# Kernel optimization log

Measured on AMD Instinct MI355X. Metric: run time of the kernel, lower is better.

## Reference

```python
import jax, jax.numpy as jnp
import numpy as np

B, N, H, NH = 4, 2048, 1024, 16
HD = H // NH  # head_dim = 64


def setup_inputs() -> dict:
    key = jax.random.key(0)
    k1, k2, k3 = jax.random.split(key, 3)
    s = 1.0 / np.sqrt(H)
    return {
        "x": jax.random.normal(k1, (B, N, H), dtype=jnp.float32),
        "w_qkv": jax.random.normal(k2, (3 * H, H), dtype=jnp.float32) * s,
        "b_qkv": jnp.zeros((3 * H,), dtype=jnp.float32),
        "w_out": jax.random.normal(k3, (H, H), dtype=jnp.float32) * s,
        "b_out": jnp.zeros((H,), dtype=jnp.float32),
    }


def reference(x, w_qkv, b_qkv, w_out, b_out):
    b, n, h = x.shape
    qkv = x @ w_qkv.T + b_qkv  # [b, n, 3h]
    q, k, v = jnp.split(qkv, 3, axis=-1)
    # [b, n, h] -> [b, nh, n, hd]
    def heads(t):
        return t.reshape(b, n, NH, HD).transpose(0, 2, 1, 3)
    q, k, v = heads(q), heads(k), heads(v)
    scale = HD ** -0.5
    dots = jnp.einsum('bhqd,bhkd->bhqk', q, k) * scale
    attn = jax.nn.softmax(dots, axis=-1)
    out = jnp.einsum('bhqk,bhkd->bhqd', attn, v)
    out = out.transpose(0, 2, 1, 3).reshape(b, n, h)
    return out @ w_out.T + b_out
```

## Files before the change

### kernel.cpp

```cpp
#include <hip/hip_runtime.h>

typedef __bf16 bf16x8 __attribute__((ext_vector_type(8)));
typedef float f32x4 __attribute__((ext_vector_type(4)));
typedef float f32x16 __attribute__((ext_vector_type(16)));
typedef unsigned int uint2v __attribute__((ext_vector_type(2)));

#define LOG2E 1.44269504088896340736f

#if __has_builtin(__builtin_amdgcn_exp2f)
#define EXP2(x) __builtin_amdgcn_exp2f(x)
#else
#define EXP2(x) exp2f(x)
#endif

static __device__ __forceinline__ unsigned short f2bf(float f) {
    unsigned int u = __builtin_bit_cast(unsigned int, f);
    u += 0x7fffu + ((u >> 16) & 1u);
    return (unsigned short)(u >> 16);
}

static __device__ __forceinline__ void plswap(unsigned int& a, unsigned int& b) {
#if __has_builtin(__builtin_amdgcn_permlane32_swap)
    uint2v r = __builtin_amdgcn_permlane32_swap(a, b, false, false);
    a = r.x; b = r.y;
#else
    asm("v_permlane32_swap_b32 %0, %1" : "+v"(a), "+v"(b));
#endif
}

static __device__ __forceinline__ float xhalf_add(float x) {
    unsigned int a = __builtin_bit_cast(unsigned int, x), b = a;
    plswap(a, b);
    return __builtin_bit_cast(float, a) + __builtin_bit_cast(float, b);
}

__global__ void cvt3_kernel(const float* __restrict__ x, const float* __restrict__ wq,
                            const float* __restrict__ wo,
                            unsigned short* __restrict__ xb, unsigned short* __restrict__ wqb,
                            unsigned short* __restrict__ wob) {
    int i = blockIdx.x * blockDim.x + threadIdx.x;
    int stride = gridDim.x * blockDim.x;
    for (; i < 3145728; i += stride) {
        const float* src;
        unsigned short* dst;
        int j;
        if (i < 2097152)      { j = i;           src = x;  dst = xb;  }
        else if (i < 2883584) { j = i - 2097152; src = wq; dst = wqb; }
        else                  { j = i - 2883584; src = wo; dst = wob; }
        float4 v = reinterpret_cast<const float4*>(src)[j];
        ushort4 o;
        o.x = f2bf(v.x); o.y = f2bf(v.y); o.z = f2bf(v.z); o.w = f2bf(v.w);
        reinterpret_cast<ushort4*>(dst)[j] = o;
    }
}

template <int MODE>
__global__ __launch_bounds__(256, 2) void gemm_bt(const unsigned short* __restrict__ A,
                                                  const unsigned short* __restrict__ B,
                                                  const float* __restrict__ bias,
                                                  void* __restrict__ Cout,
                                                  int M, int N, int K) {
    __shared__ unsigned short SH[2][2][128 * 64];
    const int tid = threadIdx.x;
    const int w = tid >> 6, lane = tid & 63;
    const int wr = w >> 1, wc = w & 1;
    const int bm0 = blockIdx.y << 7, bn0 = blockIdx.x << 7;
    const int l15 = lane & 15, l4 = lane >> 4;

    const int srow = w * 8 + (lane >> 3);
    const int gch = (lane & 7) ^ (lane >> 3);

    f32x4 acc[4][4] = {};

    auto stage = [&](int buf, int kt) {
        const int k0 = kt << 6;
        #pragma unroll
        for (int i = 0; i < 4; ++i) {
            int row = i * 32 + srow;
            const unsigned short* ga = A + (size_t)(bm0 + row) * K + k0 + gch * 8;
            __builtin_amdgcn_global_load_lds(
                (const __attribute__((address_space(1))) void*)ga,
                (__attribute__((address_space(3))) void*)&SH[buf][0][i * 2048 + w * 512],
                16, 0, 0);
            const unsigned short* gb = B + (size_t)(bn0 + row) * K + k0 + gch * 8;
            __builtin_amdgcn_global_load_lds(
                (const __attribute__((address_space(1))) void*)gb,
                (__attribute__((address_space(3))) void*)&SH[buf][1][i * 2048 + w * 512],
                16, 0, 0);
        }
    };

    const int nk = K >> 6;
    stage(0, 0);
    __syncthreads();
    int buf = 0;
    for (int kt = 0; kt < nk; ++kt) {
        if (kt + 1 < nk) stage(buf ^ 1, kt + 1);
        const unsigned short* as = &SH[buf][0][0];
        const unsigned short* bs = &SH[buf][1][0];
        #pragma unroll
        for (int s = 0; s < 2; ++s) {
            bf16x8 af[4], bfr[4];
            #pragma unroll
            for (int t = 0; t < 4; ++t) {
                int rowa = wr * 64 + t * 16 + l15;
                int cha = (s * 4 + l4) ^ (rowa & 7);
                af[t] = *(const bf16x8*)&as[rowa * 64 + cha * 8];
                int rowb = wc * 64 + t * 16 + l15;
                int chb = (s * 4 + l4) ^ (rowb & 7);
                bfr[t] = *(const bf16x8*)&bs[rowb * 64 + chb * 8];
            }
            #pragma unroll
            for (int i = 0; i < 4; ++i)
                #pragma unroll
                for (int j = 0; j < 4; ++j)
                    acc[i][j] = __builtin_amdgcn_mfma_f32_16x16x32_bf16(af[i], bfr[j], acc[i][j], 0, 0, 0);
        }
        __syncthreads();
        buf ^= 1;
    }

    if (MODE == 0) {
        unsigned short* O = (unsigned short*)Cout;
        if (bn0 >= 2048) {
            unsigned short* T = &SH[0][0][0];
            __syncthreads();
            #pragma unroll
            for (int j = 0; j < 4; ++j) {
                int cl = wc * 64 + j * 16 + l15;
                float bv = bias[bn0 + cl];
                #pragma unroll
                for (int i = 0; i < 4; ++i) {
                    int nl = wr * 64 + i * 16 + l4 * 4;
                    ushort4 pk;
                    pk.x = f2bf(acc[i][j][0] + bv);
                    pk.y = f2bf(acc[i][j][1] + bv);
                    pk.z = f2bf(acc[i][j][2] + bv);
                    pk.w = f2bf(acc[i][j][3] + bv);
                    *(ushort4*)&T[cl * 136 + nl] = pk;
                }
            }
            __syncthreads();
            const int b = bm0 >> 11, n0 = bm0 & 2047;
            const int h0 = (bn0 >> 6) & 15;
            #pragma unroll
            for (int it = 0; it < 8; ++it) {
                int dl = it * 16 + (tid >> 4);
                int ch = tid & 15;
                uint4 val = *(const uint4*)&T[dl * 136 + ch * 8];
                size_t idx = (size_t)16777216 +
                             ((size_t)((b * 16 + (h0 + (dl >> 6))) * 64 + (dl & 63))) * 2048 +
                             n0 + ch * 8;
                *(uint4*)&O[idx] = val;
            }
        } else {
            #pragma unroll
            for (int j = 0; j < 4; ++j) {
                int col = bn0 + wc * 64 + j * 16 + l15;
                float bv = bias[col];
                int which = col >> 10;
                int h = (col >> 6) & 15;
                int d = col & 63;
                #pragma unroll
                for (int i = 0; i < 4; ++i) {
                    #pragma unroll
                    for (int r = 0; r < 4; ++r) {
                        int row = bm0 + wr * 64 + i * 16 + l4 * 4 + r;
                        int b = row >> 11, n = row & 2047;
                        float v = acc[i][j][r] + bv;
                        size_t idx;
                        if (which == 0) { v *= 0.125f * LOG2E; idx = ((size_t)((b * 16 + h) * 2048 + n)) * 64 + d; }
                        else { idx = (size_t)8388608 + ((size_t)((b * 16 + h) * 2048 + n)) * 64 + d; }
                        O[idx] = f2bf(v);
                    }
                }
            }
        }
    } else {
        float* C = (float*)Cout;
        #pragma unroll
        for (int j = 0; j < 4; ++j) {
            int col = bn0 + wc * 64 + j * 16 + l15;
            float bv = bias[col];
            #pragma unroll
            for (int i = 0; i < 4; ++i) {
                #pragma unroll
                for (int r = 0; r < 4; ++r) {
                    int row = bm0 + wr * 64 + i * 16 + l4 * 4 + r;
                    C[(size_t)row * N + col] = acc[i][j][r] + bv;
                }
            }
        }
    }
}

__global__ __launch_bounds__(256, 2) void attn_kernel(const unsigned short* __restrict__ qkv,
                                                      unsigned short* __restrict__ out) {
    __shared__ unsigned short Klds[2][4096];
    __shared__ unsigned short Vlds[2][4096];

    const int tid = threadIdx.x;
    const int w = tid >> 6, lane = tid & 63;
    const int ql = lane & 31;
    const int hi = lane >> 5;
    const int id = blockIdx.x;
    const int bh = id & 63;
    const int qt = id >> 6;
    const size_t SEC = 8388608;

    const unsigned short* Q  = qkv + (size_t)bh * (2048 * 64);
    const unsigned short* Kp = qkv + SEC + (size_t)bh * (2048 * 64);
    const unsigned short* Vt = qkv + 2 * SEC + (size_t)bh * (64 * 2048);

    const int q0 = qt * 256 + w * 64;

    bf16x8 qbA[4], qbB[4];
    #pragma unroll
    for (int c = 0; c < 4; ++c) {
        qbA[c] = *(const bf16x8*)&Q[(size_t)(q0 + ql) * 64 + c * 16 + hi * 8];
        qbB[c] = *(const bf16x8*)&Q[(size_t)(q0 + 32 + ql) * 64 + c * 16 + hi * 8];
    }

    f32x16 oA0 = {}, oA1 = {}, oB0 = {}, oB1 = {};
    float lsA = 0.f, lsB = 0.f;

    const int sri = lane >> 3;
    const int sch = lane & 7;

    auto stage = [&](int buf, int tile) {
        const int kb = tile * 64;
        #pragma unroll
        for (int i = 0; i < 2; ++i) {
            const int r = w * 16 + i * 8 + sri;
            const int c = sch ^ (r & 7);
            const unsigned short* gk = Kp + (size_t)(kb + r) * 64 + c * 8;
            __builtin_amdgcn_global_load_lds(
                (const __attribute__((address_space(1))) void*)gk,
                (__attribute__((address_space(3))) void*)&Klds[buf][w * 1024 + i * 512],
                16, 0, 0);
            const unsigned short* gv = Vt + (size_t)r * 2048 + kb + c * 8;
            __builtin_amdgcn_global_load_lds(
                (const __attribute__((address_space(1))) void*)gv,
                (__attribute__((address_space(3))) void*)&Vlds[buf][w * 1024 + i * 512],
                16, 0, 0);
        }
    };

    auto softmax_block = [&](f32x16& s0, f32x16& s1, float& lsum,
                             bf16x8 (&p0)[2], bf16x8 (&p1)[2]) {
        #pragma unroll
        for (int r = 0; r < 16; ++r) s0[r] = EXP2(s0[r]);
        #pragma unroll
        for (int r = 0; r < 16; ++r) s1[r] = EXP2(s1[r]);
        float u0 = ((s0[0] + s0[1]) + (s0[2] + s0[3])) + ((s0[4] + s0[5]) + (s0[6] + s0[7]));
        float u1 = ((s0[8] + s0[9]) + (s0[10] + s0[11])) + ((s0[12] + s0[13]) + (s0[14] + s0[15]));
        float u2 = ((s1[0] + s1[1]) + (s1[2] + s1[3])) + ((s1[4] + s1[5]) + (s1[6] + s1[7]));
        float u3 = ((s1[8] + s1[9]) + (s1[10] + s1[11])) + ((s1[12] + s1[13]) + (s1[14] + s1[15]));
        float rs = (u0 + u1) + (u2 + u3);
        lsum += xhalf_add(rs);
        #pragma unroll
        for (int g = 0; g < 2; ++g) {
            unsigned int x0, x1, x2, x3;
            asm("v_cvt_pk_bf16_f32 %0, %1, %2" : "=v"(x0) : "v"(s0[8*g + 0]), "v"(s0[8*g + 1]));
            asm("v_cvt_pk_bf16_f32 %0, %1, %2" : "=v"(x1) : "v"(s0[8*g + 2]), "v"(s0[8*g + 3]));
            asm("v_cvt_pk_bf16_f32 %0, %1, %2" : "=v"(x2) : "v"(s0[8*g + 4]), "v"(s0[8*g + 5]));
            asm("v_cvt_pk_bf16_f32 %0, %1, %2" : "=v"(x3) : "v"(s0[8*g + 6]), "v"(s0[8*g + 7]));
            plswap(x0, x2);
            plswap(x1, x3);
            uint4 wds; wds.x = x0; wds.y = x1; wds.z = x2; wds.w = x3;
            p0[g] = __builtin_bit_cast(bf16x8, wds);
        }
        #pragma unroll
        for (int g = 0; g < 2; ++g) {
            unsigned int x0, x1, x2, x3;
            asm("v_cvt_pk_bf16_f32 %0, %1, %2" : "=v"(x0) : "v"(s1[8*g + 0]), "v"(s1[8*g + 1]));
            asm("v_cvt_pk_bf16_f32 %0, %1, %2" : "=v"(x1) : "v"(s1[8*g + 2]), "v"(s1[8*g + 3]));
            asm("v_cvt_pk_bf16_f32 %0, %1, %2" : "=v"(x2) : "v"(s1[8*g + 4]), "v"(s1[8*g + 5]));
            asm("v_cvt_pk_bf16_f32 %0, %1, %2" : "=v"(x3) : "v"(s1[8*g + 6]), "v"(s1[8*g + 7]));
            plswap(x0, x2);
            plswap(x1, x3);
            uint4 wds; wds.x = x0; wds.y = x1; wds.z = x2; wds.w = x3;
            p1[g] = __builtin_bit_cast(bf16x8, wds);
        }
    };

    stage(0, 0);
    __syncthreads();

    for (int t = 0; t < 32; ++t) {
        const int cur = t & 1;
        if (t + 1 < 32) stage(cur ^ 1, t + 1);

        bf16x8 k0[4], k1[4];
        #pragma unroll
        for (int mf = 0; mf < 4; ++mf) {
            int c0 = ((mf * 2 + hi) ^ (ql & 7));
            k0[mf] = *(const bf16x8*)&Klds[cur][ql * 64 + c0 * 8];
            k1[mf] = *(const bf16x8*)&Klds[cur][(32 + ql) * 64 + c0 * 8];
        }

        f32x16 sA0 = {}, sA1 = {};
        #pragma unroll
        for (int mf = 0; mf < 4; ++mf)
            sA0 = __builtin_amdgcn_mfma_f32_32x32x16_bf16(k0[mf], qbA[mf], sA0, 0, 0, 0);
        #pragma unroll
        for (int mf = 0; mf < 4; ++mf)
            sA1 = __builtin_amdgcn_mfma_f32_32x32x16_bf16(k1[mf], qbA[mf], sA1, 0, 0, 0);
        f32x16 sB0 = {}, sB1 = {};
        #pragma unroll
        for (int mf = 0; mf < 4; ++mf)
            sB0 = __builtin_amdgcn_mfma_f32_32x32x16_bf16(k0[mf], qbB[mf], sB0, 0, 0, 0);
        #pragma unroll
        for (int mf = 0; mf < 4; ++mf)
            sB1 = __builtin_amdgcn_mfma_f32_32x32x16_bf16(k1[mf], qbB[mf], sB1, 0, 0, 0);

        bf16x8 v0[4], v1[4];
        #pragma unroll
        for (int ks = 0; ks < 4; ++ks) {
            int c0 = ((ks * 2 + hi) ^ (ql & 7));
            v0[ks] = *(const bf16x8*)&Vlds[cur][ql * 64 + c0 * 8];
            v1[ks] = *(const bf16x8*)&Vlds[cur][(32 + ql) * 64 + c0 * 8];
        }

        bf16x8 pA0[2], pA1[2], pB0[2], pB1[2];
        softmax_block(sA0, sA1, lsA, pA0, pA1);
        softmax_block(sB0, sB1, lsB, pB0, pB1);

        oA0 = __builtin_amdgcn_mfma_f32_32x32x16_bf16(v0[0], pA0[0], oA0, 0, 0, 0);
        oA0 = __builtin_amdgcn_mfma_f32_32x32x16_bf16(v0[1], pA0[1], oA0, 0, 0, 0);
        oA0 = __builtin_amdgcn_mfma_f32_32x32x16_bf16(v0[2], pA1[0], oA0, 0, 0, 0);
        oA0 = __builtin_amdgcn_mfma_f32_32x32x16_bf16(v0[3], pA1[1], oA0, 0, 0, 0);
        oA1 = __builtin_amdgcn_mfma_f32_32x32x16_bf16(v1[0], pA0[0], oA1, 0, 0, 0);
        oA1 = __builtin_amdgcn_mfma_f32_32x32x16_bf16(v1[1], pA0[1], oA1, 0, 0, 0);
        oA1 = __builtin_amdgcn_mfma_f32_32x32x16_bf16(v1[2], pA1[0], oA1, 0, 0, 0);
        oA1 = __builtin_amdgcn_mfma_f32_32x32x16_bf16(v1[3], pA1[1], oA1, 0, 0, 0);
        oB0 = __builtin_amdgcn_mfma_f32_32x32x16_bf16(v0[0], pB0[0], oB0, 0, 0, 0);
        oB0 = __builtin_amdgcn_mfma_f32_32x32x16_bf16(v0[1], pB0[1], oB0, 0, 0, 0);
        oB0 = __builtin_amdgcn_mfma_f32_32x32x16_bf16(v0[2], pB1[0], oB0, 0, 0, 0);
        oB0 = __builtin_amdgcn_mfma_f32_32x32x16_bf16(v0[3], pB1[1], oB0, 0, 0, 0);
        oB1 = __builtin_amdgcn_mfma_f32_32x32x16_bf16(v1[0], pB0[0], oB1, 0, 0, 0);
        oB1 = __builtin_amdgcn_mfma_f32_32x32x16_bf16(v1[1], pB0[1], oB1, 0, 0, 0);
        oB1 = __builtin_amdgcn_mfma_f32_32x32x16_bf16(v1[2], pB1[0], oB1, 0, 0, 0);
        oB1 = __builtin_amdgcn_mfma_f32_32x32x16_bf16(v1[3], pB1[1], oB1, 0, 0, 0);

        __syncthreads();
    }

    const int b = bh >> 4, h = bh & 15;
    {
        const float inv = 1.0f / lsA;
        const int n = q0 + ql;
        unsigned short* obase = out + ((size_t)(b * 2048 + n)) * 1024 + h * 64;
        #pragma unroll
        for (int g = 0; g < 4; ++g) {
            int d0 = 8 * g + 4 * hi;
            ushort4 w0, w1;
            w0.x = f2bf(oA0[4 * g + 0] * inv);
            w0.y = f2bf(oA0[4 * g + 1] * inv);
            w0.z = f2bf(oA0[4 * g + 2] * inv);
            w0.w = f2bf(oA0[4 * g + 3] * inv);
            *(ushort4*)(obase + d0) = w0;
            w1.x = f2bf(oA1[4 * g + 0] * inv);
            w1.y = f2bf(oA1[4 * g + 1] * inv);
            w1.z = f2bf(oA1[4 * g + 2] * inv);
            w1.w = f2bf(oA1[4 * g + 3] * inv);
            *(ushort4*)(obase + 32 + d0) = w1;
        }
    }
    {
        const float inv = 1.0f / lsB;
        const int n = q0 + 32 + ql;
        unsigned short* obase = out + ((size_t)(b * 2048 + n)) * 1024 + h * 64;
        #pragma unroll
        for (int g = 0; g < 4; ++g) {
            int d0 = 8 * g + 4 * hi;
            ushort4 w0, w1;
            w0.x = f2bf(oB0[4 * g + 0] * inv);
            w0.y = f2bf(oB0[4 * g + 1] * inv);
            w0.z = f2bf(oB0[4 * g + 2] * inv);
            w0.w = f2bf(oB0[4 * g + 3] * inv);
            *(ushort4*)(obase + d0) = w0;
            w1.x = f2bf(oB1[4 * g + 0] * inv);
            w1.y = f2bf(oB1[4 * g + 1] * inv);
            w1.z = f2bf(oB1[4 * g + 2] * inv);
            w1.w = f2bf(oB1[4 * g + 3] * inv);
            *(ushort4*)(obase + 32 + d0) = w1;
        }
    }
}

extern "C" void kernel_launch(void* const* d_in, const int* in_sizes, int n_in,
                              void* d_out, int out_size, void* d_ws, size_t ws_size,
                              hipStream_t stream) {
    (void)in_sizes; (void)n_in; (void)out_size; (void)ws_size;
    const float* x     = (const float*)d_in[0];
    const float* w_qkv = (const float*)d_in[1];
    const float* b_qkv = (const float*)d_in[2];
    const float* w_out = (const float*)d_in[3];
    const float* b_out = (const float*)d_in[4];

    unsigned short* ws = (unsigned short*)d_ws;
    unsigned short* xb    = ws;
    unsigned short* wqkvb = ws + 8388608;
    unsigned short* woutb = ws + 11534336;
    unsigned short* qkvb  = ws + 12582912;

    cvt3_kernel<<<dim3(2048), dim3(256), 0, stream>>>(x, w_qkv, w_out, xb, wqkvb, woutb);

    gemm_bt<0><<<dim3(24, 64), dim3(256), 0, stream>>>(xb, wqkvb, b_qkv, (void*)qkvb, 8192, 3072, 1024);

    attn_kernel<<<dim3(512), dim3(256), 0, stream>>>(qkvb, xb);

    gemm_bt<1><<<dim3(8, 64), dim3(256), 0, stream>>>(xb, woutb, b_out, d_out, 8192, 1024, 1024);
}
```

Measured before the change: 176.0 us.

## Split attention work across 8 waves with 32 query rows each

The attention block grows from 256 to 512 threads, so each wave handles 32 query rows instead of 64. Each wave holds half the Q fragments and accumulators, which lowers register pressure and allows more waves per CU for latency hiding. K/V staging is spread over 8 waves with one load each. The cost is that every wave reads the full K/V tile from LDS for half the math, doubling LDS read traffic per MFMA, and the barrier now covers more waves.

New measurement: 178.5 us. Within noise of the previous version (+1.4%).

```diff
diff --git a/kernel.cpp b/kernel.cpp
--- a/kernel.cpp
+++ b/kernel.cpp
@@ -194,7 +194,7 @@
     }
 }
 
-__global__ __launch_bounds__(256, 2) void attn_kernel(const unsigned short* __restrict__ qkv,
+__global__ __launch_bounds__(512, 4) void attn_kernel(const unsigned short* __restrict__ qkv,
                                                       unsigned short* __restrict__ out) {
     __shared__ unsigned short Klds[2][4096];
     __shared__ unsigned short Vlds[2][4096];
@@ -212,42 +212,66 @@
     const unsigned short* Kp = qkv + SEC + (size_t)bh * (2048 * 64);
     const unsigned short* Vt = qkv + 2 * SEC + (size_t)bh * (64 * 2048);
 
-    const int q0 = qt * 256 + w * 64;
-
-    bf16x8 qbA[4], qbB[4];
+    const int q0 = qt * 256 + w * 32;
+
+    bf16x8 qb[4];
     #pragma unroll
-    for (int c = 0; c < 4; ++c) {
-        qbA[c] = *(const bf16x8*)&Q[(size_t)(q0 + ql) * 64 + c * 16 + hi * 8];
-        qbB[c] = *(const bf16x8*)&Q[(size_t)(q0 + 32 + ql) * 64 + c * 16 + hi * 8];
-    }
-
-    f32x16 oA0 = {}, oA1 = {}, oB0 = {}, oB1 = {};
-    float lsA = 0.f, lsB = 0.f;
+    for (int c = 0; c < 4; ++c)
+        qb[c] = *(const bf16x8*)&Q[(size_t)(q0 + ql) * 64 + c * 16 + hi * 8];
+
+    f32x16 o0 = {}, o1 = {};
+    float ls = 0.f;
 
     const int sri = lane >> 3;
     const int sch = lane & 7;
 
     auto stage = [&](int buf, int tile) {
         const int kb = tile * 64;
-        #pragma unroll
-        for (int i = 0; i < 2; ++i) {
-            const int r = w * 16 + i * 8 + sri;
-            const int c = sch ^ (r & 7);
-            const unsigned short* gk = Kp + (size_t)(kb + r) * 64 + c * 8;
-            __builtin_amdgcn_global_load_lds(
-                (const __attribute__((address_space(1))) void*)gk,
-                (__attribute__((address_space(3))) void*)&Klds[buf][w * 1024 + i * 512],
-                16, 0, 0);
-            const unsigned short* gv = Vt + (size_t)r * 2048 + kb + c * 8;
-            __builtin_amdgcn_global_load_lds(
-                (const __attribute__((address_space(1))) void*)gv,
-                (__attribute__((address_space(3))) void*)&Vlds[buf][w * 1024 + i * 512],
-                16, 0, 0);
-        }
+        const int r = w * 8 + sri;
+        const int c = sch ^ (r & 7);
+        const unsigned short* gk = Kp + (size_t)(kb + r) * 64 + c * 8;
+        __builtin_amdgcn_global_load_lds(
+            (const __attribute__((address_space(1))) void*)gk,
+            (__attribute__((address_space(3))) void*)&Klds[buf][w * 512],
+            16, 0, 0);
+        const unsigned short* gv = Vt + (size_t)r * 2048 + kb + c * 8;
+        __builtin_amdgcn_global_load_lds(
+            (const __attribute__((address_space(1))) void*)gv,
+            (__attribute__((address_space(3))) void*)&Vlds[buf][w * 512],
+            16, 0, 0);
     };
 
-    auto softmax_block = [&](f32x16& s0, f32x16& s1, float& lsum,
-                             bf16x8 (&p0)[2], bf16x8 (&p1)[2]) {
+    stage(0, 0);
+    __syncthreads();
+
+    for (int t = 0; t < 32; ++t) {
+        const int cur = t & 1;
+        if (t + 1 < 32) stage(cur ^ 1, t + 1);
+
+        bf16x8 k0[4], k1[4];
+        #pragma unroll
+        for (int mf = 0; mf < 4; ++mf) {
+            int c0 = ((mf * 2 + hi) ^ (ql & 7));
+            k0[mf] = *(const bf16x8*)&Klds[cur][ql * 64 + c0 * 8];
+            k1[mf] = *(const bf16x8*)&Klds[cur][(32 + ql) * 64 + c0 * 8];
+        }
+
+        f32x16 s0 = {}, s1 = {};
+        #pragma unroll
+        for (int mf = 0; mf < 4; ++mf)
+            s0 = __builtin_amdgcn_mfma_f32_32x32x16_bf16(k0[mf], qb[mf], s0, 0, 0, 0);
+        #pragma unroll
+        for (int mf = 0; mf < 4; ++mf)
+            s1 = __builtin_amdgcn_mfma_f32_32x32x16_bf16(k1[mf], qb[mf], s1, 0, 0, 0);
+
+        bf16x8 v0[4], v1[4];
+        #pragma unroll
+        for (int ks = 0; ks < 4; ++ks) {
+            int c0 = ((ks * 2 + hi) ^ (ql & 7));
+            v0[ks] = *(const bf16x8*)&Vlds[cur][ql * 64 + c0 * 8];
+            v1[ks] = *(const bf16x8*)&Vlds[cur][(32 + ql) * 64 + c0 * 8];
+        }
+
         #pragma unroll
         for (int r = 0; r < 16; ++r) s0[r] = EXP2(s0[r]);
         #pragma unroll
@@ -257,7 +281,9 @@
         float u2 = ((s1[0] + s1[1]) + (s1[2] + s1[3])) + ((s1[4] + s1[5]) + (s1[6] + s1[7]));
         float u3 = ((s1[8] + s1[9]) + (s1[10] + s1[11])) + ((s1[12] + s1[13]) + (s1[14] + s1[15]));
         float rs = (u0 + u1) + (u2 + u3);
-        lsum += xhalf_add(rs);
+        ls += xhalf_add(rs);
+
+        bf16x8 p0[2], p1[2];
         #pragma unroll
         for (int g = 0; g < 2; ++g) {
             unsigned int x0, x1, x2, x3;
@@ -282,110 +308,37 @@
             uint4 wds; wds.x = x0; wds.y = x1; wds.z = x2; wds.w = x3;
             p1[g] = __builtin_bit_cast(bf16x8, wds);
         }
-    };
-
-    stage(0, 0);
-    __syncthreads();
-
-    for (int t = 0; t < 32; ++t) {
-        const int cur = t & 1;
-        if (t + 1 < 32) stage(cur ^ 1, t + 1);
-
-        bf16x8 k0[4], k1[4];
-        #pragma unroll
-        for (int mf = 0; mf < 4; ++mf) {
-            int c0 = ((mf * 2 + hi) ^ (ql & 7));
-            k0[mf] = *(const bf16x8*)&Klds[cur][ql * 64 + c0 * 8];
-            k1[mf] = *(const bf16x8*)&Klds[cur][(32 + ql) * 64 + c0 * 8];
-        }
-
-        f32x16 sA0 = {}, sA1 = {};
-        #pragma unroll
-        for (int mf = 0; mf < 4; ++mf)
-            sA0 = __builtin_amdgcn_mfma_f32_32x32x16_bf16(k0[mf], qbA[mf], sA0, 0, 0, 0);
-        #pragma unroll
-        for (int mf = 0; mf < 4; ++mf)
-            sA1 = __builtin_amdgcn_mfma_f32_32x32x16_bf16(k1[mf], qbA[mf], sA1, 0, 0, 0);
-        f32x16 sB0 = {}, sB1 = {};
-        #pragma unroll
-        for (int mf = 0; mf < 4; ++mf)
-            sB0 = __builtin_amdgcn_mfma_f32_32x32x16_bf16(k0[mf], qbB[mf], sB0, 0, 0, 0);
-        #pragma unroll
-        for (int mf = 0; mf < 4; ++mf)
-            sB1 = __builtin_amdgcn_mfma_f32_32x32x16_bf16(k1[mf], qbB[mf], sB1, 0, 0, 0);
-
-        bf16x8 v0[4], v1[4];
-        #pragma unroll
-        for (int ks = 0; ks < 4; ++ks) {
-            int c0 = ((ks * 2 + hi) ^ (ql & 7));
-            v0[ks] = *(const bf16x8*)&Vlds[cur][ql * 64 + c0 * 8];
-            v1[ks] = *(const bf16x8*)&Vlds[cur][(32 + ql) * 64 + c0 * 8];
-        }
-
-        bf16x8 pA0[2], pA1[2], pB0[2], pB1[2];
-        softmax_block(sA0, sA1, lsA, pA0, pA1);
-        softmax_block(sB0, sB1, lsB, pB0, pB1);
-
-        oA0 = __builtin_amdgcn_mfma_f32_32x32x16_bf16(v0[0], pA0[0], oA0, 0, 0, 0);
-        oA0 = __builtin_amdgcn_mfma_f32_32x32x16_bf16(v0[1], pA0[1], oA0, 0, 0, 0);
-        oA0 = __builtin_amdgcn_mfma_f32_32x32x16_bf16(v0[2], pA1[0], oA0, 0, 0, 0);
-        oA0 = __builtin_amdgcn_mfma_f32_32x32x16_bf16(v0[3], pA1[1], oA0, 0, 0, 0);
-        oA1 = __builtin_amdgcn_mfma_f32_32x32x16_bf16(v1[0], pA0[0], oA1, 0, 0, 0);
-        oA1 = __builtin_amdgcn_mfma_f32_32x32x16_bf16(v1[1], pA0[1], oA1, 0, 0, 0);
-        oA1 = __builtin_amdgcn_mfma_f32_32x32x16_bf16(v1[2], pA1[0], oA1, 0, 0, 0);
-        oA1 = __builtin_amdgcn_mfma_f32_32x32x16_bf16(v1[3], pA1[1], oA1, 0, 0, 0);
-        oB0 = __builtin_amdgcn_mfma_f32_32x32x16_bf16(v0[0], pB0[0], oB0, 0, 0, 0);
-        oB0 = __builtin_amdgcn_mfma_f32_32x32x16_bf16(v0[1], pB0[1], oB0, 0, 0, 0);
-        oB0 = __builtin_amdgcn_mfma_f32_32x32x16_bf16(v0[2], pB1[0], oB0, 0, 0, 0);
-        oB0 = __builtin_amdgcn_mfma_f32_32x32x16_bf16(v0[3], pB1[1], oB0, 0, 0, 0);
-        oB1 = __builtin_amdgcn_mfma_f32_32x32x16_bf16(v1[0], pB0[0], oB1, 0, 0, 0);
-        oB1 = __builtin_amdgcn_mfma_f32_32x32x16_bf16(v1[1], pB0[1], oB1, 0, 0, 0);
-        oB1 = __builtin_amdgcn_mfma_f32_32x32x16_bf16(v1[2], pB1[0], oB1, 0, 0, 0);
-        oB1 = __builtin_amdgcn_mfma_f32_32x32x16_bf16(v1[3], pB1[1], oB1, 0, 0, 0);
+
+        o0 = __builtin_amdgcn_mfma_f32_32x32x16_bf16(v0[0], p0[0], o0, 0, 0, 0);
+        o0 = __builtin_amdgcn_mfma_f32_32x32x16_bf16(v0[1], p0[1], o0, 0, 0, 0);
+        o0 = __builtin_amdgcn_mfma_f32_32x32x16_bf16(v0[2], p1[0], o0, 0, 0, 0);
+        o0 = __builtin_amdgcn_mfma_f32_32x32x16_bf16(v0[3], p1[1], o0, 0, 0, 0);
+        o1 = __builtin_amdgcn_mfma_f32_32x32x16_bf16(v1[0], p0[0], o1, 0, 0, 0);
+        o1 = __builtin_amdgcn_mfma_f32_32x32x16_bf16(v1[1], p0[1], o1, 0, 0, 0);
+        o1 = __builtin_amdgcn_mfma_f32_32x32x16_bf16(v1[2], p1[0], o1, 0, 0, 0);
+        o1 = __builtin_amdgcn_mfma_f32_32x32x16_bf16(v1[3], p1[1], o1, 0, 0, 0);
 
         __syncthreads();
     }
 
     const int b = bh >> 4, h = bh & 15;
-    {
-        const float inv = 1.0f / lsA;
-        const int n = q0 + ql;
-        unsigned short* obase = out + ((size_t)(b * 2048 + n)) * 1024 + h * 64;
-        #pragma unroll
-        for (int g = 0; g < 4; ++g) {
-            int d0 = 8 * g + 4 * hi;
-            ushort4 w0, w1;
-            w0.x = f2bf(oA0[4 * g + 0] * inv);
-            w0.y = f2bf(oA0[4 * g + 1] * inv);
-            w0.z = f2bf(oA0[4 * g + 2] * inv);
-            w0.w = f2bf(oA0[4 * g + 3] * inv);
-            *(ushort4*)(obase + d0) = w0;
-            w1.x = f2bf(oA1[4 * g + 0] * inv);
-            w1.y = f2bf(oA1[4 * g + 1] * inv);
-            w1.z = f2bf(oA1[4 * g + 2] * inv);
-            w1.w = f2bf(oA1[4 * g + 3] * inv);
-            *(ushort4*)(obase + 32 + d0) = w1;
-        }
-    }
-    {
-        const float inv = 1.0f / lsB;
-        const int n = q0 + 32 + ql;
-        unsigned short* obase = out + ((size_t)(b * 2048 + n)) * 1024 + h * 64;
-        #pragma unroll
-        for (int g = 0; g < 4; ++g) {
-            int d0 = 8 * g + 4 * hi;
-            ushort4 w0, w1;
-            w0.x = f2bf(oB0[4 * g + 0] * inv);
-            w0.y = f2bf(oB0[4 * g + 1] * inv);
-            w0.z = f2bf(oB0[4 * g + 2] * inv);
-            w0.w = f2bf(oB0[4 * g + 3] * inv);
-            *(ushort4*)(obase + d0) = w0;
-            w1.x = f2bf(oB1[4 * g + 0] * inv);
-            w1.y = f2bf(oB1[4 * g + 1] * inv);
-            w1.z = f2bf(oB1[4 * g + 2] * inv);
-            w1.w = f2bf(oB1[4 * g + 3] * inv);
-            *(ushort4*)(obase + 32 + d0) = w1;
-        }
+    const float inv = 1.0f / ls;
+    const int n = q0 + ql;
+    unsigned short* obase = out + ((size_t)(b * 2048 + n)) * 1024 + h * 64;
+    #pragma unroll
+    for (int g = 0; g < 4; ++g) {
+        int d0 = 8 * g + 4 * hi;
+        ushort4 w0, w1;
+        w0.x = f2bf(o0[4 * g + 0] * inv);
+        w0.y = f2bf(o0[4 * g + 1] * inv);
+        w0.z = f2bf(o0[4 * g + 2] * inv);
+        w0.w = f2bf(o0[4 * g + 3] * inv);
+        *(ushort4*)(obase + d0) = w0;
+        w1.x = f2bf(o1[4 * g + 0] * inv);
+        w1.y = f2bf(o1[4 * g + 1] * inv);
+        w1.z = f2bf(o1[4 * g + 2] * inv);
+        w1.w = f2bf(o1[4 * g + 3] * inv);
+        *(ushort4*)(obase + 32 + d0) = w1;
     }
 }
 
@@ -409,7 +362,7 @@
 
     gemm_bt<0><<<dim3(24, 64), dim3(256), 0, stream>>>(xb, wqkvb, b_qkv, (void*)qkvb, 8192, 3072, 1024);
 
-    attn_kernel<<<dim3(512), dim3(256), 0, stream>>>(qkvb, xb);
+    attn_kernel<<<dim3(512), dim3(512), 0, stream>>>(qkvb, xb);
 
     gemm_bt<1><<<dim3(8, 64), dim3(256), 0, stream>>>(xb, woutb, b_out, d_out, 8192, 1024, 1024);
 }
```
